# Optimization experiments

Measured on AMD Instinct MI355X. Metric: run time of the kernel, lower is better.

Reference implementation:

```python
import jax, jax.numpy as jnp
import numpy as np

B, S, D, H = 2, 2048, 768, 12
DK = D // H


def setup_inputs() -> dict:
    key = jax.random.key(0)
    ks = jax.random.split(key, 10)
    sc = 0.02
    return {
        "k": jax.random.normal(ks[0], (B, S, D), jnp.float32),
        "q": jax.random.normal(ks[1], (B, S, D), jnp.float32),
        "v": jax.random.normal(ks[2], (B, S, D), jnp.float32),
        "mask": jnp.ones((B, 1, S, S), jnp.int32),
        "wq": jax.random.normal(ks[3], (D, D), jnp.float32) * sc,
        "bq": jnp.zeros((D,), jnp.float32),
        "wk": jax.random.normal(ks[4], (D, D), jnp.float32) * sc,
        "bk": jnp.zeros((D,), jnp.float32),
        "wv": jax.random.normal(ks[5], (D, D), jnp.float32) * sc,
        "bv": jnp.zeros((D,), jnp.float32),
        "wo": jax.random.normal(ks[6], (D, D), jnp.float32) * sc,
        "bo": jnp.zeros((D,), jnp.float32),
    }


def reference(k, q, v, mask, wq, bq, wk, bk, wv, bv, wo, bo):
    # Linear projections (torch Linear: x @ W^T + b)
    query = q @ wq.T + bq
    key_ = k @ wk.T + bk
    value = v @ wv.T + bv
    # [B,S,D] -> [B,H,S,DK]
    def split_heads(x):
        return x.reshape(B, S, H, DK).transpose(0, 2, 1, 3)
    Q, K, V = split_heads(query), split_heads(key_), split_heads(value)
    # NOTE: original masked_fill result is discarded -> mask is a no-op.
    scores = jnp.einsum("bhqd,bhkd->bhqk", Q, K) / jnp.sqrt(jnp.float32(DK))
    attn = jax.nn.softmax(scores, axis=-1)  # dropout p=0.0 -> identity
    out = jnp.einsum("bhqk,bhkd->bhqd", attn, V)
    out = out.transpose(0, 2, 1, 3).reshape(B, S, D)
    return out @ wo.T + bo
```

## Files before the change

kernel.cpp:

```cpp
#include <hip/hip_runtime.h>
#include <hip/hip_bf16.h>

#define B_  2
#define S_  2048
#define D_  768
#define H_  12
#define DK_ 64
#define NX_ (B_*S_*D_)
#define NW_ (D_*D_)
#define CSC 0.18033688011112042f

typedef __attribute__((ext_vector_type(8))) short  bf16x8;
typedef __attribute__((ext_vector_type(4))) float  f32x4;

__device__ __forceinline__ unsigned short f2bf(float f) {
    unsigned int u = __float_as_uint(f);
    u += 0x7fffu + ((u >> 16) & 1u);
    return (unsigned short)(u >> 16);
}

__device__ __forceinline__ unsigned pack_bf2(float a, float b) {
    const unsigned ua = __float_as_uint(a) + 0x8000u;
    const unsigned ub = __float_as_uint(b) + 0x8000u;
    return __builtin_amdgcn_perm(ub, ua, 0x07060302u);
}

__device__ __forceinline__ void async_cp16(const unsigned short* g,
                                           const unsigned short* lds_uniform_base) {
    __builtin_amdgcn_global_load_lds(
        (const __attribute__((address_space(1))) unsigned int*)(uintptr_t)g,
        (__attribute__((address_space(3))) unsigned int*)(unsigned int)(uintptr_t)lds_uniform_base,
        16, 0, 0);
}

struct CvtArgs { const float* s[7]; };

__global__ __launch_bounds__(256) void cvt_all(CvtArgs a,
                                               unsigned short* __restrict__ Xsw,
                                               unsigned short* __restrict__ Wsw) {
    const int bx = blockIdx.x;
    int y, inner;
    if (bx < 4608) { y = bx / 1536;       inner = bx % 1536; }
    else           { y = 3 + (bx - 4608) / 288; inner = (bx - 4608) % 288; }
    const int idx = inner * 256 + threadIdx.x;
    const int n = idx / 96;
    const int g = idx % 96;
    const float* src = a.s[y];
    const float zs = (y == 3) ? CSC : 1.0f;
    const float4 f0 = *(const float4*)(src + (long)n * D_ + g * 8);
    const float4 f1 = *(const float4*)(src + (long)n * D_ + g * 8 + 4);
    unsigned short o[8] = {f2bf(f0.x*zs), f2bf(f0.y*zs), f2bf(f0.z*zs), f2bf(f0.w*zs),
                           f2bf(f1.x*zs), f2bf(f1.y*zs), f2bf(f1.z*zs), f2bf(f1.w*zs)};
    const int kdst = (g >> 3) * 64 + (((g & 7) ^ (n & 7)) * 8);
    unsigned short* dst = (y >= 3) ? (Wsw + (long)(y - 3) * NW_) : (Xsw + (long)y * NX_);
    *(uint4*)(dst + (long)n * D_ + kdst) = *(const uint4*)o;
}

struct QkvArgs { const float* bias[3]; unsigned short* out[3]; };

__global__ __launch_bounds__(256, 2) void gemm_qkv(QkvArgs args,
                                                   const unsigned short* __restrict__ Xsw,
                                                   const unsigned short* __restrict__ Wsw) {
    __shared__ __align__(16) unsigned short smem[17408];
    unsigned short* As = smem;
    unsigned short* Bs = smem + 8192;

    const int t    = threadIdx.x;
    const int wave = t >> 6;
    const int lane = t & 63;
    const int l16  = lane & 15;
    const int quad = lane >> 4;
    const int wm   = wave >> 1, wn = wave & 1;
    const int m0   = blockIdx.x * 128;
    const int zz   = blockIdx.y / 6;
    const int nb   = blockIdx.y % 6;
    const int n0   = nb * 128;

    const unsigned short* Ap = Xsw + (long)zz * NX_;
    const unsigned short* Wp = Wsw + (long)zz * NW_;

    f32x4 acc[4][4];
#pragma unroll
    for (int s = 0; s < 4; s++)
#pragma unroll
        for (int j = 0; j < 4; j++) acc[s][j] = (f32x4){0.f, 0.f, 0.f, 0.f};

    const int lrow = lane >> 3;
    const int lcg  = lane & 7;

    for (int k0 = 0; k0 < D_; k0 += 64) {
        __syncthreads();
#pragma unroll
        for (int i = 0; i < 4; i++) {
            const int chunk = wave * 4 + i;
            async_cp16(Ap + (long)(m0 + chunk * 8 + lrow) * D_ + k0 + lcg * 8,
                       As + chunk * 512);
        }
#pragma unroll
        for (int i = 0; i < 4; i++) {
            const int chunk = wave * 4 + i;
            async_cp16(Wp + (long)(n0 + chunk * 8 + lrow) * D_ + k0 + lcg * 8,
                       Bs + chunk * 512);
        }
        __syncthreads();
#pragma unroll
        for (int ks = 0; ks < 2; ks++) {
            const int cg = ks * 4 + quad;
            bf16x8 af[4], bf[4];
#pragma unroll
            for (int s = 0; s < 4; s++) {
                const int r = wm * 64 + s * 16 + l16;
                af[s] = *(const bf16x8*)&As[r * 64 + ((cg ^ (r & 7)) * 8)];
            }
#pragma unroll
            for (int j = 0; j < 4; j++) {
                const int r = wn * 64 + j * 16 + l16;
                bf[j] = *(const bf16x8*)&Bs[r * 64 + ((cg ^ (r & 7)) * 8)];
            }
#pragma unroll
            for (int s = 0; s < 4; s++)
#pragma unroll
                for (int j = 0; j < 4; j++)
                    acc[s][j] = __builtin_amdgcn_mfma_f32_16x16x32_bf16(af[s], bf[j], acc[s][j], 0, 0, 0);
        }
    }
    __syncthreads();

    const int b     = m0 >> 11;
    const int sbase = m0 & (S_ - 1);
    const float zs  = (zz == 0) ? CSC : 1.0f;
    float bv[4];
#pragma unroll
    for (int j = 0; j < 4; j++) bv[j] = args.bias[zz][n0 + wn * 64 + j * 16 + l16] * zs;

    if (zz < 2) {
        unsigned short* Ls = smem;
#pragma unroll
        for (int s = 0; s < 4; s++)
#pragma unroll
            for (int j = 0; j < 4; j++)
#pragma unroll
                for (int r = 0; r < 4; r++)
                    Ls[(wm * 64 + s * 16 + quad * 4 + r) * 136 + wn * 64 + j * 16 + l16] =
                        f2bf(acc[s][j][r] + bv[j]);
        __syncthreads();
        const int row  = t >> 1;
        const int half = t & 1;
        unsigned short* Op = args.out[zz];
#pragma unroll
        for (int i = 0; i < 8; i++) {
            const int col  = half * 64 + i * 8;
            const int head = nb * 2 + half;
            const uint4 v = *(const uint4*)&Ls[row * 136 + col];
            *(uint4*)(Op + ((long)(b * H_ + head) * S_ + sbase + row) * DK_ + (col & 63)) = v;
        }
    } else {
        unsigned short* Ls = smem;
#pragma unroll
        for (int s = 0; s < 4; s++)
#pragma unroll
            for (int j = 0; j < 4; j++)
#pragma unroll
                for (int r = 0; r < 4; r++) {
                    const int dk  = j * 16 + l16;
                    const int pos = wm * 64 + (quad * 4 + r) * 4 + s;
                    Ls[wn * 8704 + dk * 136 + pos] = f2bf(acc[s][j][r] + bv[j]);
                }
        __syncthreads();
        const int rowIdx = t >> 1;
        const int hh = rowIdx >> 6, dk = rowIdx & 63;
        const int half = t & 1;
        unsigned short* Op = args.out[2];
#pragma unroll
        for (int i = 0; i < 8; i++) {
            const int col = half * 64 + i * 8;
            const uint4 v = *(const uint4*)&Ls[hh * 8704 + dk * 136 + col];
            const int head = nb * 2 + hh;
            *(uint4*)(Op + ((long)(b * H_ + head) * DK_ + dk) * S_ + sbase + col) = v;
        }
    }
}

__global__ __launch_bounds__(256, 3) void attn_kernel(
    const unsigned short* __restrict__ Q, const unsigned short* __restrict__ K,
    const unsigned short* __restrict__ Vt, unsigned short* __restrict__ Ao)
{
    const int t    = threadIdx.x;
    const int wave = t >> 6;
    const int lane = t & 63;
    const int l16  = lane & 15;
    const int quad = lane >> 4;
    const int qtile = blockIdx.x;
    const int bh    = blockIdx.y;

    const unsigned short* Qp = Q  + (long)bh * S_ * DK_;
    const unsigned short* Kp = K  + (long)bh * S_ * DK_;
    const unsigned short* Vp = Vt + (long)bh * DK_ * S_;

    __shared__ __align__(16) unsigned short smem[23040];

    bf16x8 qfrag[2];
    {
        const long qoff = (long)(qtile * 64 + wave * 16 + l16) * DK_ + quad * 8;
        qfrag[0] = *(const bf16x8*)(Qp + qoff);
        qfrag[1] = *(const bf16x8*)(Qp + qoff + 32);
    }
    unsigned short* Ps = smem + 18432;

    const int srow = t >> 2;
    const int scg  = (t & 3) * 16;
    uint4 kreg[2], vreg[2];
    {
        const unsigned short* gk = Kp + (long)srow * DK_ + scg;
        const unsigned short* gv = Vp + (long)srow * S_ + scg;
        kreg[0] = *(const uint4*)gk;  kreg[1] = *(const uint4*)(gk + 8);
        vreg[0] = *(const uint4*)gv;  vreg[1] = *(const uint4*)(gv + 8);
    }
    *(uint4*)&smem[srow * 72 + scg]            = kreg[0];
    *(uint4*)&smem[srow * 72 + scg + 8]        = kreg[1];
    *(uint4*)&smem[9216 + srow * 72 + scg]     = vreg[0];
    *(uint4*)&smem[9216 + srow * 72 + scg + 8] = vreg[1];

    f32x4 oacc[4];
#pragma unroll
    for (int j = 0; j < 4; j++) oacc[j] = (f32x4){0.f, 0.f, 0.f, 0.f};
    float lsum[4] = {0.f, 0.f, 0.f, 0.f};

    for (int it = 0; it < 32; ++it) {
        const int co = (it & 1) * 4608;
        const int no = ((it & 1) ^ 1) * 4608;
        __syncthreads();
        const unsigned short* Ks = smem + co;
        const unsigned short* Vs = smem + 9216 + co;

        if (it < 31) {
            const int kv0 = (it + 1) * 64;
            const unsigned short* gk = Kp + (long)(kv0 + srow) * DK_ + scg;
            const unsigned short* gv = Vp + (long)srow * S_ + kv0 + scg;
            kreg[0] = *(const uint4*)gk;  kreg[1] = *(const uint4*)(gk + 8);
            vreg[0] = *(const uint4*)gv;  vreg[1] = *(const uint4*)(gv + 8);
        }

        f32x4 sacc[4];
#pragma unroll
        for (int j = 0; j < 4; j++) sacc[j] = (f32x4){0.f, 0.f, 0.f, 0.f};
#pragma unroll
        for (int ks = 0; ks < 2; ks++)
#pragma unroll
            for (int j = 0; j < 4; j++) {
                const bf16x8 bf = *(const bf16x8*)&Ks[(j * 16 + l16) * 72 + ks * 32 + quad * 8];
                sacc[j] = __builtin_amdgcn_mfma_f32_16x16x32_bf16(qfrag[ks], bf, sacc[j], 0, 0, 0);
            }

#pragma unroll
        for (int r = 0; r < 4; r++) {
            const float p0 = exp2f(sacc[0][r]);
            const float p1 = exp2f(sacc[1][r]);
            const float p2 = exp2f(sacc[2][r]);
            const float p3 = exp2f(sacc[3][r]);
            lsum[r] += (p0 + p1) + (p2 + p3);
            uint2 pk = {pack_bf2(p0, p1), pack_bf2(p2, p3)};
            *(uint2*)&Ps[(wave * 16 + quad * 4 + r) * 72 + l16 * 4] = pk;
        }

#pragma unroll
        for (int ks = 0; ks < 2; ks++) {
            const bf16x8 pf = *(const bf16x8*)&Ps[(wave * 16 + l16) * 72 + ks * 32 + quad * 8];
#pragma unroll
            for (int j = 0; j < 4; j++) {
                const bf16x8 vf = *(const bf16x8*)&Vs[(j * 16 + l16) * 72 + ks * 32 + quad * 8];
                oacc[j] = __builtin_amdgcn_mfma_f32_16x16x32_bf16(pf, vf, oacc[j], 0, 0, 0);
            }
        }

        if (it < 31) {
            *(uint4*)&smem[no + srow * 72 + scg]            = kreg[0];
            *(uint4*)&smem[no + srow * 72 + scg + 8]        = kreg[1];
            *(uint4*)&smem[9216 + no + srow * 72 + scg]     = vreg[0];
            *(uint4*)&smem[9216 + no + srow * 72 + scg + 8] = vreg[1];
        }
    }

#pragma unroll
    for (int r = 0; r < 4; r++) {
#pragma unroll
        for (int off = 1; off < 16; off <<= 1)
            lsum[r] += __shfl_xor(lsum[r], off, 64);
        lsum[r] = 1.f / lsum[r];
    }

    __syncthreads();
#pragma unroll
    for (int j = 0; j < 4; j++)
#pragma unroll
        for (int r = 0; r < 4; r++)
            Ps[(wave * 16 + quad * 4 + r) * 72 + j * 16 + l16] =
                f2bf(oacc[j][r] * lsum[r]);

    const int b = bh / H_, h = bh % H_;
    const int row = t >> 2;
    const int c0  = (t & 3) * 16;
    const int qrow = qtile * 64 + row;
    const int key  = qrow & 7;
    const uint4 v0 = *(const uint4*)&Ps[row * 72 + c0];
    const uint4 v1 = *(const uint4*)&Ps[row * 72 + c0 + 8];
    const int g8 = c0 >> 3;
    unsigned short* dst = Ao + (long)(b * S_ + qrow) * D_ + h * DK_;
    *(uint4*)(dst + ((g8 ^ key) * 8))       = v0;
    *(uint4*)(dst + (((g8 + 1) ^ key) * 8)) = v1;
}

__global__ __launch_bounds__(256, 2) void gemm_out(
    const unsigned short* __restrict__ A, const unsigned short* __restrict__ Wsw,
    const float* __restrict__ bias, float* __restrict__ Out)
{
    __shared__ __align__(16) unsigned short smem[17408];
    unsigned short* As = smem;
    unsigned short* Bs = smem + 8192;

    const int t    = threadIdx.x;
    const int wave = t >> 6;
    const int lane = t & 63;
    const int l16  = lane & 15;
    const int quad = lane >> 4;
    const int wm   = wave >> 1, wn = wave & 1;
    const int m0   = blockIdx.x * 128;
    const int n0   = blockIdx.y * 128;

    f32x4 acc[4][4];
#pragma unroll
    for (int s = 0; s < 4; s++)
#pragma unroll
        for (int j = 0; j < 4; j++) acc[s][j] = (f32x4){0.f, 0.f, 0.f, 0.f};

    const int lrow = lane >> 3;
    const int lcg  = lane & 7;

    for (int k0 = 0; k0 < D_; k0 += 64) {
        __syncthreads();
#pragma unroll
        for (int i = 0; i < 4; i++) {
            const int chunk = wave * 4 + i;
            async_cp16(A + (long)(m0 + chunk * 8 + lrow) * D_ + k0 + lcg * 8,
                       As + chunk * 512);
        }
#pragma unroll
        for (int i = 0; i < 4; i++) {
            const int chunk = wave * 4 + i;
            async_cp16(Wsw + (long)(n0 + chunk * 8 + lrow) * D_ + k0 + lcg * 8,
                       Bs + chunk * 512);
        }
        __syncthreads();
#pragma unroll
        for (int ks = 0; ks < 2; ks++) {
            const int cg = ks * 4 + quad;
            bf16x8 af[4], bf[4];
#pragma unroll
            for (int s = 0; s < 4; s++) {
                const int r = wm * 64 + s * 16 + l16;
                af[s] = *(const bf16x8*)&As[r * 64 + ((cg ^ (r & 7)) * 8)];
            }
#pragma unroll
            for (int j = 0; j < 4; j++) {
                const int r = wn * 64 + j * 16 + l16;
                bf[j] = *(const bf16x8*)&Bs[r * 64 + ((cg ^ (r & 7)) * 8)];
            }
#pragma unroll
            for (int s = 0; s < 4; s++)
#pragma unroll
                for (int j = 0; j < 4; j++)
                    acc[s][j] = __builtin_amdgcn_mfma_f32_16x16x32_bf16(af[s], bf[j], acc[s][j], 0, 0, 0);
        }
    }

    float bv[4];
#pragma unroll
    for (int j = 0; j < 4; j++) bv[j] = bias[n0 + wn * 64 + j * 16 + l16];

    float* fl = (float*)smem;
#pragma unroll
    for (int h = 0; h < 2; h++) {
        __syncthreads();
        if (wn == h) {
#pragma unroll
            for (int s = 0; s < 4; s++)
#pragma unroll
                for (int j = 0; j < 4; j++)
#pragma unroll
                    for (int r = 0; r < 4; r++)
                        fl[(wm * 64 + s * 16 + quad * 4 + r) * 67 + j * 16 + l16] =
                            acc[s][j][r] + bv[j];
        }
        __syncthreads();
        const int row = t >> 1, c0 = (t & 1) * 32;
#pragma unroll
        for (int i = 0; i < 8; i++) {
            const float4 v = *(const float4*)&fl[row * 67 + c0 + i * 4];
            *(float4*)(Out + (long)(m0 + row) * D_ + n0 + h * 64 + c0 + i * 4) = v;
        }
    }
}

extern "C" void kernel_launch(void* const* d_in, const int* in_sizes, int n_in,
                              void* d_out, int out_size, void* d_ws, size_t ws_size,
                              hipStream_t stream) {
    const float* k_in = (const float*)d_in[0];
    const float* q_in = (const float*)d_in[1];
    const float* v_in = (const float*)d_in[2];
    const float* wq = (const float*)d_in[4];
    const float* bq = (const float*)d_in[5];
    const float* wk = (const float*)d_in[6];
    const float* bk = (const float*)d_in[7];
    const float* wv = (const float*)d_in[8];
    const float* bv = (const float*)d_in[9];
    const float* wo = (const float*)d_in[10];
    const float* bo = (const float*)d_in[11];

    unsigned short* ws = (unsigned short*)d_ws;
    unsigned short* Wsw = ws;
    unsigned short* Qb  = Wsw + 4ll * NW_;
    unsigned short* Kb  = Qb + (long)NX_;
    unsigned short* Vt  = Kb + (long)NX_;
    unsigned short* Xsw = Vt + (long)NX_;
    unsigned short* Ao  = Xsw;

    CvtArgs ca;
    ca.s[0] = q_in; ca.s[1] = k_in; ca.s[2] = v_in;
    ca.s[3] = wq;   ca.s[4] = wk;   ca.s[5] = wv;  ca.s[6] = wo;
    cvt_all<<<dim3(5760), 256, 0, stream>>>(ca, Xsw, Wsw);

    QkvArgs qa;
    qa.bias[0] = bq; qa.bias[1] = bk; qa.bias[2] = bv;
    qa.out[0] = Qb;  qa.out[1] = Kb;  qa.out[2] = Vt;
    gemm_qkv<<<dim3(32, 18), 256, 0, stream>>>(qa, Xsw, Wsw);

    attn_kernel<<<dim3(S_ / 64, B_ * H_), 256, 0, stream>>>(Qb, Kb, Vt, Ao);

    gemm_out<<<dim3(32, 6), 256, 0, stream>>>(Ao, Wsw + 3ll * NW_, bo, (float*)d_out);
}
```

Before: 219.0 us.

## Shrink output GEMM tiles, widen conversion work per thread, tweak occupancy

The output projection GEMM moves from 128x128 to 64x64 tiles. That raises the grid from 192 to 768 blocks so more CUs are busy, and lets the epilogue write in one pass. The conversion kernel now handles 16 elements per thread with half the blocks. gemm_qkv's launch bound goes from 2 to 3 blocks per CU, and attention advances its K/V pointers incrementally instead of recomputing addresses. Smaller tiles cost operand reuse in the output GEMM, and the higher occupancy target may force register spills.

```diff
diff --git a/kernel.cpp b/kernel.cpp
--- a/kernel.cpp
+++ b/kernel.cpp
@@ -40,25 +40,34 @@
                                                unsigned short* __restrict__ Wsw) {
     const int bx = blockIdx.x;
     int y, inner;
-    if (bx < 4608) { y = bx / 1536;       inner = bx % 1536; }
-    else           { y = 3 + (bx - 4608) / 288; inner = (bx - 4608) % 288; }
+    if (bx < 2304) { y = bx / 768;             inner = bx % 768; }
+    else           { y = 3 + (bx - 2304) / 144; inner = (bx - 2304) % 144; }
     const int idx = inner * 256 + threadIdx.x;
-    const int n = idx / 96;
-    const int g = idx % 96;
-    const float* src = a.s[y];
+    const int n  = idx / 48;
+    const int g2 = idx % 48;
+    const float* src = a.s[y] + (long)n * D_ + g2 * 16;
     const float zs = (y == 3) ? CSC : 1.0f;
-    const float4 f0 = *(const float4*)(src + (long)n * D_ + g * 8);
-    const float4 f1 = *(const float4*)(src + (long)n * D_ + g * 8 + 4);
-    unsigned short o[8] = {f2bf(f0.x*zs), f2bf(f0.y*zs), f2bf(f0.z*zs), f2bf(f0.w*zs),
-                           f2bf(f1.x*zs), f2bf(f1.y*zs), f2bf(f1.z*zs), f2bf(f1.w*zs)};
-    const int kdst = (g >> 3) * 64 + (((g & 7) ^ (n & 7)) * 8);
-    unsigned short* dst = (y >= 3) ? (Wsw + (long)(y - 3) * NW_) : (Xsw + (long)y * NX_);
-    *(uint4*)(dst + (long)n * D_ + kdst) = *(const uint4*)o;
+    unsigned short o[16];
+#pragma unroll
+    for (int i = 0; i < 4; i++) {
+        const float4 f = *(const float4*)(src + i * 4);
+        o[i*4+0] = f2bf(f.x*zs); o[i*4+1] = f2bf(f.y*zs);
+        o[i*4+2] = f2bf(f.z*zs); o[i*4+3] = f2bf(f.w*zs);
+    }
+    unsigned short* dst = (y >= 3) ? (Wsw + (long)(y - 3) * NW_ + (long)n * D_)
+                                   : (Xsw + (long)y * NX_ + (long)n * D_);
+    const int key = n & 7;
+#pragma unroll
+    for (int h = 0; h < 2; h++) {
+        const int g8 = g2 * 2 + h;
+        const int kdst = (g8 >> 3) * 64 + (((g8 & 7) ^ key) * 8);
+        *(uint4*)(dst + kdst) = *(const uint4*)&o[h * 8];
+    }
 }
 
 struct QkvArgs { const float* bias[3]; unsigned short* out[3]; };
 
-__global__ __launch_bounds__(256, 2) void gemm_qkv(QkvArgs args,
+__global__ __launch_bounds__(256, 3) void gemm_qkv(QkvArgs args,
                                                    const unsigned short* __restrict__ Xsw,
                                                    const unsigned short* __restrict__ Wsw) {
     __shared__ __align__(16) unsigned short smem[17408];
@@ -198,6 +207,7 @@
     const unsigned short* Vp = Vt + (long)bh * DK_ * S_;
 
     __shared__ __align__(16) unsigned short smem[23040];
+    unsigned short* Ps = smem + 18432;
 
     bf16x8 qfrag[2];
     {
@@ -205,17 +215,15 @@
         qfrag[0] = *(const bf16x8*)(Qp + qoff);
         qfrag[1] = *(const bf16x8*)(Qp + qoff + 32);
     }
-    unsigned short* Ps = smem + 18432;
 
     const int srow = t >> 2;
     const int scg  = (t & 3) * 16;
     uint4 kreg[2], vreg[2];
-    {
-        const unsigned short* gk = Kp + (long)srow * DK_ + scg;
-        const unsigned short* gv = Vp + (long)srow * S_ + scg;
-        kreg[0] = *(const uint4*)gk;  kreg[1] = *(const uint4*)(gk + 8);
-        vreg[0] = *(const uint4*)gv;  vreg[1] = *(const uint4*)(gv + 8);
-    }
+    const unsigned short* gk = Kp + (long)srow * DK_ + scg;
+    const unsigned short* gv = Vp + (long)srow * S_ + scg;
+    kreg[0] = *(const uint4*)gk;  kreg[1] = *(const uint4*)(gk + 8);
+    vreg[0] = *(const uint4*)gv;  vreg[1] = *(const uint4*)(gv + 8);
+    gk += 64 * DK_;  gv += 64;
     *(uint4*)&smem[srow * 72 + scg]            = kreg[0];
     *(uint4*)&smem[srow * 72 + scg + 8]        = kreg[1];
     *(uint4*)&smem[9216 + srow * 72 + scg]     = vreg[0];
@@ -234,11 +242,9 @@
         const unsigned short* Vs = smem + 9216 + co;
 
         if (it < 31) {
-            const int kv0 = (it + 1) * 64;
-            const unsigned short* gk = Kp + (long)(kv0 + srow) * DK_ + scg;
-            const unsigned short* gv = Vp + (long)srow * S_ + kv0 + scg;
             kreg[0] = *(const uint4*)gk;  kreg[1] = *(const uint4*)(gk + 8);
             vreg[0] = *(const uint4*)gv;  vreg[1] = *(const uint4*)(gv + 8);
+            gk += 64 * DK_;  gv += 64;
         }
 
         f32x4 sacc[4];
@@ -310,13 +316,13 @@
     *(uint4*)(dst + (((g8 + 1) ^ key) * 8)) = v1;
 }
 
-__global__ __launch_bounds__(256, 2) void gemm_out(
+__global__ __launch_bounds__(256, 4) void gemm_out(
     const unsigned short* __restrict__ A, const unsigned short* __restrict__ Wsw,
     const float* __restrict__ bias, float* __restrict__ Out)
 {
-    __shared__ __align__(16) unsigned short smem[17408];
+    __shared__ __align__(16) unsigned short smem[8704];
     unsigned short* As = smem;
-    unsigned short* Bs = smem + 8192;
+    unsigned short* Bs = smem + 4096;
 
     const int t    = threadIdx.x;
     const int wave = t >> 6;
@@ -324,14 +330,14 @@
     const int l16  = lane & 15;
     const int quad = lane >> 4;
     const int wm   = wave >> 1, wn = wave & 1;
-    const int m0   = blockIdx.x * 128;
-    const int n0   = blockIdx.y * 128;
-
-    f32x4 acc[4][4];
-#pragma unroll
-    for (int s = 0; s < 4; s++)
-#pragma unroll
-        for (int j = 0; j < 4; j++) acc[s][j] = (f32x4){0.f, 0.f, 0.f, 0.f};
+    const int m0   = blockIdx.x * 64;
+    const int n0   = blockIdx.y * 64;
+
+    f32x4 acc[2][2];
+#pragma unroll
+    for (int s = 0; s < 2; s++)
+#pragma unroll
+        for (int j = 0; j < 2; j++) acc[s][j] = (f32x4){0.f, 0.f, 0.f, 0.f};
 
     const int lrow = lane >> 3;
     const int lcg  = lane & 7;
@@ -339,14 +345,14 @@
     for (int k0 = 0; k0 < D_; k0 += 64) {
         __syncthreads();
 #pragma unroll
-        for (int i = 0; i < 4; i++) {
-            const int chunk = wave * 4 + i;
+        for (int i = 0; i < 2; i++) {
+            const int chunk = wave * 2 + i;
             async_cp16(A + (long)(m0 + chunk * 8 + lrow) * D_ + k0 + lcg * 8,
                        As + chunk * 512);
         }
 #pragma unroll
-        for (int i = 0; i < 4; i++) {
-            const int chunk = wave * 4 + i;
+        for (int i = 0; i < 2; i++) {
+            const int chunk = wave * 2 + i;
             async_cp16(Wsw + (long)(n0 + chunk * 8 + lrow) * D_ + k0 + lcg * 8,
                        Bs + chunk * 512);
         }
@@ -354,50 +360,45 @@
 #pragma unroll
         for (int ks = 0; ks < 2; ks++) {
             const int cg = ks * 4 + quad;
-            bf16x8 af[4], bf[4];
-#pragma unroll
-            for (int s = 0; s < 4; s++) {
-                const int r = wm * 64 + s * 16 + l16;
+            bf16x8 af[2], bf[2];
+#pragma unroll
+            for (int s = 0; s < 2; s++) {
+                const int r = wm * 32 + s * 16 + l16;
                 af[s] = *(const bf16x8*)&As[r * 64 + ((cg ^ (r & 7)) * 8)];
             }
 #pragma unroll
-            for (int j = 0; j < 4; j++) {
-                const int r = wn * 64 + j * 16 + l16;
+            for (int j = 0; j < 2; j++) {
+                const int r = wn * 32 + j * 16 + l16;
                 bf[j] = *(const bf16x8*)&Bs[r * 64 + ((cg ^ (r & 7)) * 8)];
             }
 #pragma unroll
-            for (int s = 0; s < 4; s++)
-#pragma unroll
-                for (int j = 0; j < 4; j++)
+            for (int s = 0; s < 2; s++)
+#pragma unroll
+                for (int j = 0; j < 2; j++)
                     acc[s][j] = __builtin_amdgcn_mfma_f32_16x16x32_bf16(af[s], bf[j], acc[s][j], 0, 0, 0);
         }
     }
 
-    float bv[4];
-#pragma unroll
-    for (int j = 0; j < 4; j++) bv[j] = bias[n0 + wn * 64 + j * 16 + l16];
-
+    float bv[2];
+#pragma unroll
+    for (int j = 0; j < 2; j++) bv[j] = bias[n0 + wn * 32 + j * 16 + l16];
+
+    __syncthreads();
     float* fl = (float*)smem;
 #pragma unroll
-    for (int h = 0; h < 2; h++) {
-        __syncthreads();
-        if (wn == h) {
-#pragma unroll
-            for (int s = 0; s < 4; s++)
-#pragma unroll
-                for (int j = 0; j < 4; j++)
-#pragma unroll
-                    for (int r = 0; r < 4; r++)
-                        fl[(wm * 64 + s * 16 + quad * 4 + r) * 67 + j * 16 + l16] =
-                            acc[s][j][r] + bv[j];
-        }
-        __syncthreads();
-        const int row = t >> 1, c0 = (t & 1) * 32;
-#pragma unroll
-        for (int i = 0; i < 8; i++) {
-            const float4 v = *(const float4*)&fl[row * 67 + c0 + i * 4];
-            *(float4*)(Out + (long)(m0 + row) * D_ + n0 + h * 64 + c0 + i * 4) = v;
-        }
+    for (int s = 0; s < 2; s++)
+#pragma unroll
+        for (int j = 0; j < 2; j++)
+#pragma unroll
+            for (int r = 0; r < 4; r++)
+                fl[(wm * 32 + s * 16 + quad * 4 + r) * 67 + wn * 32 + j * 16 + l16] =
+                    acc[s][j][r] + bv[j];
+    __syncthreads();
+    const int row = t >> 2, c0 = (t & 3) * 16;
+#pragma unroll
+    for (int i = 0; i < 4; i++) {
+        const float4 v = *(const float4*)&fl[row * 67 + c0 + i * 4];
+        *(float4*)(Out + (long)(m0 + row) * D_ + n0 + c0 + i * 4) = v;
     }
 }
 
@@ -427,7 +428,7 @@
     CvtArgs ca;
     ca.s[0] = q_in; ca.s[1] = k_in; ca.s[2] = v_in;
     ca.s[3] = wq;   ca.s[4] = wk;   ca.s[5] = wv;  ca.s[6] = wo;
-    cvt_all<<<dim3(5760), 256, 0, stream>>>(ca, Xsw, Wsw);
+    cvt_all<<<dim3(2880), 256, 0, stream>>>(ca, Xsw, Wsw);
 
     QkvArgs qa;
     qa.bias[0] = bq; qa.bias[1] = bk; qa.bias[2] = bv;
@@ -436,5 +437,5 @@
 
     attn_kernel<<<dim3(S_ / 64, B_ * H_), 256, 0, stream>>>(Qb, Kb, Vt, Ao);
 
-    gemm_out<<<dim3(32, 6), 256, 0, stream>>>(Ao, Wsw + 3ll * NW_, bo, (float*)d_out);
-}
+    gemm_out<<<dim3(64, 12), 256, 0, stream>>>(Ao, Wsw + 3ll * NW_, bo, (float*)d_out);
+}
```

Result: faster. 214.5 us (-2.1%).
